# Kernel tuning notes

Hardware: AMD Instinct MI355X
Metric: run time of the kernel (lower is better)

The kernel has to match this reference:

```python
import jax, jax.numpy as jnp
import numpy as np


def setup_inputs() -> dict:
    key = jax.random.key(0)
    k1, k2 = jax.random.split(key)
    batch, cw_dim = 4096, 1024
    dim_embedding, book_size = 8, 256
    dim_codes = cw_dim // dim_embedding  # 128
    x = jax.random.normal(k1, (batch, cw_dim), dtype=jnp.float32)
    codebook = jax.random.normal(k2, (dim_codes, book_size, dim_embedding), dtype=jnp.float32)
    return {"x": x, "codebook": codebook}


def reference(x, codebook):
    # Faithful JAX version of VQVAE.quantise:
    #   pairwise squared distance -> argmin -> gather embeddings -> one-hot scatter
    C, K, D = codebook.shape          # dim_codes, book_size, dim_embedding
    B = x.shape[0]
    xr = x.reshape(B, C, D)           # [B, C, D] (= view(batch*dim_codes, 1, D))
    x2 = jnp.sum(xr * xr, axis=-1)                       # [B, C]
    c2 = jnp.sum(codebook * codebook, axis=-1)           # [C, K]
    dist = x2[..., None] - 2.0 * jnp.einsum('bcd,ckd->bck', xr, codebook) + c2[None]
    idx = jnp.argmin(dist, axis=-1)                      # [B, C]
    # gather nearest codebook entry per code slot
    cw_embed = codebook[jnp.arange(C)[None, :], idx]     # [B, C, D]
    cw_embed = cw_embed.reshape(B, C * D)                # [B, cw_dim]
    # one-hot scatter of selected indices
    one_hot_idx = jax.nn.one_hot(idx, K, dtype=jnp.float32)  # [B, C, K]
    return cw_embed, one_hot_idx
```

## Files before the change

kernel.cpp:

```cpp
#include <hip/hip_runtime.h>


constexpr int B_    = 4096;
constexpr int C_    = 128;
constexpr int K_    = 256;
constexpr int D_    = 8;
constexpr int TPB   = 256;
constexpr int BPT   = 4;
constexpr int BTILE = TPB * BPT;

__global__ __launch_bounds__(TPB, 2) void vq_argmin(
    const float* __restrict__ x,
    const float* __restrict__ cb,
    int* __restrict__ idx_out)
{
    __shared__ double s_cbd[K_ * D_];
    __shared__ double s_c2d[K_];

    const int c     = blockIdx.x;
    const int btile = blockIdx.y;
    const int tid   = threadIdx.x;

    {
        const float4* gcb = (const float4*)(cb + (size_t)c * (K_ * D_));
        const float4 v0 = gcb[tid];
        const float4 v1 = gcb[tid + TPB];
        const int i0 = tid * 4, i1 = (tid + TPB) * 4;
        s_cbd[i0 + 0] = (double)v0.x; s_cbd[i0 + 1] = (double)v0.y;
        s_cbd[i0 + 2] = (double)v0.z; s_cbd[i0 + 3] = (double)v0.w;
        s_cbd[i1 + 0] = (double)v1.x; s_cbd[i1 + 1] = (double)v1.y;
        s_cbd[i1 + 2] = (double)v1.z; s_cbd[i1 + 3] = (double)v1.w;
    }
    __syncthreads();

    {
        const double* v = s_cbd + tid * D_;
        double s = 0.0;
        #pragma unroll
        for (int d = 0; d < D_; ++d) s = fma(v[d], v[d], s);
        s_c2d[tid] = s;
    }
    __syncthreads();

    double xd[BPT][D_];
    #pragma unroll
    for (int j = 0; j < BPT; ++j) {
        const int b = btile * BTILE + j * TPB + tid;
        const float4* xp = (const float4*)(x + (size_t)b * (C_ * D_) + c * D_);
        const float4 a = xp[0];
        const float4 h = xp[1];
        xd[j][0] = (double)a.x; xd[j][1] = (double)a.y;
        xd[j][2] = (double)a.z; xd[j][3] = (double)a.w;
        xd[j][4] = (double)h.x; xd[j][5] = (double)h.y;
        xd[j][6] = (double)h.z; xd[j][7] = (double)h.w;
    }

    double best[BPT];
    int    bidx[BPT];
    #pragma unroll
    for (int j = 0; j < BPT; ++j) { best[j] = 1.0e300; bidx[j] = 0; }

    for (int k = 0; k < K_; ++k) {
        double cd[D_];
        #pragma unroll
        for (int d = 0; d < D_; ++d) cd[d] = s_cbd[k * D_ + d];
        const double c2k = s_c2d[k];
        #pragma unroll
        for (int j = 0; j < BPT; ++j) {
            double dot = xd[j][0] * cd[0];
            #pragma unroll
            for (int d = 1; d < D_; ++d) dot = fma(xd[j][d], cd[d], dot);
            const double score = fma(-2.0, dot, c2k);
            const bool lt = score < best[j];
            best[j] = lt ? score : best[j];
            bidx[j] = lt ? k : bidx[j];
        }
    }

    #pragma unroll
    for (int j = 0; j < BPT; ++j) {
        const int b = btile * BTILE + j * TPB + tid;
        idx_out[(size_t)b * C_ + c] = bidx[j];
    }
}

constexpr int GRID2 = 2048;
constexpr int RPB   = (B_ * C_) / GRID2;

__global__ __launch_bounds__(TPB, 4) void vq_write(
    const int*   __restrict__ idx,
    const float* __restrict__ cb,
    float* __restrict__ out_embed,
    float* __restrict__ out_onehot)
{
    const int tid  = threadIdx.x;
    const int lane = tid & 63;
    const int wave = tid >> 6;
    const int blk  = blockIdx.x;

    const int rowbase = blk * RPB + wave * 64;
    const int myk = idx[rowbase + lane];
    const int e0 = lane * 4;
    #pragma unroll 4
    for (int i = 0; i < 64; ++i) {
        const int k = __builtin_amdgcn_readlane(myk, i);
        float4 v;
        v.x = (k == e0    ) ? 1.f : 0.f;
        v.y = (k == e0 + 1) ? 1.f : 0.f;
        v.z = (k == e0 + 2) ? 1.f : 0.f;
        v.w = (k == e0 + 3) ? 1.f : 0.f;
        ((float4*)(out_onehot + (size_t)(rowbase + i) * K_))[lane] = v;
    }

    const size_t pbase = (size_t)blk * RPB;
    #pragma unroll
    for (int i = 0; i < 2; ++i) {
        const int    f    = i * TPB + tid;
        const int    pl   = f >> 1;
        const int    half = f & 1;
        const size_t pair = pbase + pl;
        const int    c    = (int)(pair & (C_ - 1));
        const int    k    = idx[pair];
        const float4 val  = ((const float4*)(cb + ((size_t)c * K_ + k) * D_))[half];
        ((float4*)(out_embed + pbase * D_))[f] = val;
    }
}

extern "C" void kernel_launch(void* const* d_in, const int* in_sizes, int n_in,
                              void* d_out, int out_size, void* d_ws, size_t ws_size,
                              hipStream_t stream) {
    const float* x  = (const float*)d_in[0];
    const float* cb = (const float*)d_in[1];
    float* out        = (float*)d_out;
    float* out_embed  = out;
    float* out_onehot = out + (size_t)B_ * C_ * D_;
    int*   idx_ws     = (int*)d_ws;

    dim3 grid1(C_, B_ / BTILE);
    vq_argmin<<<grid1, TPB, 0, stream>>>(x, cb, idx_ws);

    vq_write<<<GRID2, TPB, 0, stream>>>(idx_ws, cb, out_embed, out_onehot);
}
```

Measured before the change: 617.8 us.

## Screen argmin in fp32 and recheck near-tie pairs in fp64

Replaces the all-fp64 distance search with an fp32 pass that tracks both the best and second-best scores. Pairs whose margin falls under a small threshold are flagged in the sign bit, and a new fix-up kernel recomputes only those pairs in fp64 using a wave-wide reduction. The output writes also switch to nontemporal stores. This removes most of the slow fp64 arithmetic, at the cost of an extra launch and a threshold that could miss ties if fp32 error exceeds it.

```diff
diff --git a/kernel.cpp b/kernel.cpp
--- a/kernel.cpp
+++ b/kernel.cpp
@@ -1,21 +1,26 @@
 #include <hip/hip_runtime.h>
 
 
-constexpr int B_    = 4096;
-constexpr int C_    = 128;
-constexpr int K_    = 256;
-constexpr int D_    = 8;
-constexpr int TPB   = 256;
-constexpr int BPT   = 4;
-constexpr int BTILE = TPB * BPT;
-
-__global__ __launch_bounds__(TPB, 2) void vq_argmin(
+constexpr int B_  = 4096;
+constexpr int C_  = 128;
+constexpr int K_  = 256;
+constexpr int D_  = 8;
+constexpr int TPB = 256;
+constexpr int NP  = B_ * C_;
+
+typedef float  vf4 __attribute__((ext_vector_type(4)));
+
+constexpr int   BPT1   = 2;
+constexpr int   BTILE1 = TPB * BPT1;
+constexpr float TAU2   = 1.0e-3f;
+
+__global__ __launch_bounds__(TPB, 4) void vq_screen(
     const float* __restrict__ x,
     const float* __restrict__ cb,
     int* __restrict__ idx_out)
 {
-    __shared__ double s_cbd[K_ * D_];
-    __shared__ double s_c2d[K_];
+    __shared__ float s_cbf[K_ * D_];
+    __shared__ float s_c2f[K_];
 
     const int c     = blockIdx.x;
     const int btile = blockIdx.y;
@@ -23,69 +28,126 @@
 
     {
         const float4* gcb = (const float4*)(cb + (size_t)c * (K_ * D_));
-        const float4 v0 = gcb[tid];
-        const float4 v1 = gcb[tid + TPB];
-        const int i0 = tid * 4, i1 = (tid + TPB) * 4;
-        s_cbd[i0 + 0] = (double)v0.x; s_cbd[i0 + 1] = (double)v0.y;
-        s_cbd[i0 + 2] = (double)v0.z; s_cbd[i0 + 3] = (double)v0.w;
-        s_cbd[i1 + 0] = (double)v1.x; s_cbd[i1 + 1] = (double)v1.y;
-        s_cbd[i1 + 2] = (double)v1.z; s_cbd[i1 + 3] = (double)v1.w;
+        ((float4*)s_cbf)[tid]       = gcb[tid];
+        ((float4*)s_cbf)[tid + TPB] = gcb[tid + TPB];
     }
     __syncthreads();
-
     {
-        const double* v = s_cbd + tid * D_;
-        double s = 0.0;
+        const float* v = s_cbf + tid * D_;
+        float s = 0.f;
         #pragma unroll
-        for (int d = 0; d < D_; ++d) s = fma(v[d], v[d], s);
-        s_c2d[tid] = s;
+        for (int d = 0; d < D_; ++d) s = fmaf(v[d], v[d], s);
+        s_c2f[tid] = s;
     }
     __syncthreads();
 
-    double xd[BPT][D_];
-    #pragma unroll
-    for (int j = 0; j < BPT; ++j) {
-        const int b = btile * BTILE + j * TPB + tid;
+    float xf[BPT1][D_];
+    #pragma unroll
+    for (int j = 0; j < BPT1; ++j) {
+        const int b = btile * BTILE1 + j * TPB + tid;
         const float4* xp = (const float4*)(x + (size_t)b * (C_ * D_) + c * D_);
         const float4 a = xp[0];
         const float4 h = xp[1];
-        xd[j][0] = (double)a.x; xd[j][1] = (double)a.y;
-        xd[j][2] = (double)a.z; xd[j][3] = (double)a.w;
-        xd[j][4] = (double)h.x; xd[j][5] = (double)h.y;
-        xd[j][6] = (double)h.z; xd[j][7] = (double)h.w;
-    }
-
-    double best[BPT];
-    int    bidx[BPT];
-    #pragma unroll
-    for (int j = 0; j < BPT; ++j) { best[j] = 1.0e300; bidx[j] = 0; }
-
+        xf[j][0] = a.x; xf[j][1] = a.y; xf[j][2] = a.z; xf[j][3] = a.w;
+        xf[j][4] = h.x; xf[j][5] = h.y; xf[j][6] = h.z; xf[j][7] = h.w;
+    }
+
+    float s1[BPT1], s2[BPT1];
+    int   k1[BPT1];
+    #pragma unroll
+    for (int j = 0; j < BPT1; ++j) { s1[j] = 3.4e38f; s2[j] = 3.4e38f; k1[j] = 0; }
+
+    const float4* scb4 = (const float4*)s_cbf;
+    #pragma unroll 2
     for (int k = 0; k < K_; ++k) {
-        double cd[D_];
+        const float4 clo = scb4[k * 2];
+        const float4 chi = scb4[k * 2 + 1];
+        const float  c2k = s_c2f[k];
         #pragma unroll
-        for (int d = 0; d < D_; ++d) cd[d] = s_cbd[k * D_ + d];
-        const double c2k = s_c2d[k];
-        #pragma unroll
-        for (int j = 0; j < BPT; ++j) {
-            double dot = xd[j][0] * cd[0];
+        for (int j = 0; j < BPT1; ++j) {
+            float dot = xf[j][0] * clo.x;
+            dot = fmaf(xf[j][1], clo.y, dot);
+            dot = fmaf(xf[j][2], clo.z, dot);
+            dot = fmaf(xf[j][3], clo.w, dot);
+            dot = fmaf(xf[j][4], chi.x, dot);
+            dot = fmaf(xf[j][5], chi.y, dot);
+            dot = fmaf(xf[j][6], chi.z, dot);
+            dot = fmaf(xf[j][7], chi.w, dot);
+            const float score = fmaf(-2.f, dot, c2k);
+            s2[j] = fminf(s2[j], fmaxf(score, s1[j]));
+            const bool lt = score < s1[j];
+            k1[j] = lt ? k : k1[j];
+            s1[j] = lt ? score : s1[j];
+        }
+    }
+
+    #pragma unroll
+    for (int j = 0; j < BPT1; ++j) {
+        const int b = btile * BTILE1 + j * TPB + tid;
+        const bool amb = (s2[j] - s1[j]) <= TAU2;
+        idx_out[(size_t)b * C_ + c] = k1[j] | (amb ? (1 << 31) : 0);
+    }
+}
+
+constexpr int FIXBLKS = 256;
+
+__global__ __launch_bounds__(TPB, 4) void vq_fix(
+    const float* __restrict__ x,
+    const float* __restrict__ cb,
+    int* __restrict__ idx)
+{
+    const int lane   = threadIdx.x & 63;
+    const int gwave  = (blockIdx.x * TPB + threadIdx.x) >> 6;
+    const int nwaves = (FIXBLKS * TPB) >> 6;
+
+    for (int base = gwave * 64; base < NP; base += nwaves * 64) {
+        const int v = idx[base + lane];
+        unsigned long long mask = __ballot(v < 0);
+        while (mask) {
+            const int src = (int)__ffsll((long long)mask) - 1;
+            mask &= mask - 1;
+            const int pair = base + src;
+            const int b = pair >> 7;
+            const int c = pair & (C_ - 1);
+
+            const float* xp = x  + (size_t)b * (C_ * D_) + c * D_;
+            const float* cp = cb + (size_t)c * (K_ * D_);
+
+            double xd[D_];
             #pragma unroll
-            for (int d = 1; d < D_; ++d) dot = fma(xd[j][d], cd[d], dot);
-            const double score = fma(-2.0, dot, c2k);
-            const bool lt = score < best[j];
-            best[j] = lt ? score : best[j];
-            bidx[j] = lt ? k : bidx[j];
+            for (int d = 0; d < D_; ++d) xd[d] = (double)xp[d];
+
+            double best = 1.0e300;
+            int    bk   = 0;
+            #pragma unroll
+            for (int t = 0; t < 4; ++t) {
+                const int k = lane * 4 + t;
+                const float* cv = cp + k * D_;
+                double cd[D_];
+                #pragma unroll
+                for (int d = 0; d < D_; ++d) cd[d] = (double)cv[d];
+                double c2k = 0.0;
+                #pragma unroll
+                for (int d = 0; d < D_; ++d) c2k = fma(cd[d], cd[d], c2k);
+                double dot = xd[0] * cd[0];
+                #pragma unroll
+                for (int d = 1; d < D_; ++d) dot = fma(xd[d], cd[d], dot);
+                const double score = fma(-2.0, dot, c2k);
+                if (score < best) { best = score; bk = k; }
+            }
+            #pragma unroll
+            for (int off = 32; off >= 1; off >>= 1) {
+                const double ob  = __shfl_down(best, off);
+                const int    obk = __shfl_down(bk,   off);
+                if (ob < best) { best = ob; bk = obk; }
+            }
+            if (lane == 0) idx[pair] = bk;
         }
     }
-
-    #pragma unroll
-    for (int j = 0; j < BPT; ++j) {
-        const int b = btile * BTILE + j * TPB + tid;
-        idx_out[(size_t)b * C_ + c] = bidx[j];
-    }
-}
-
-constexpr int GRID2 = 2048;
-constexpr int RPB   = (B_ * C_) / GRID2;
+}
+
+constexpr int GRID3 = 2048;
+constexpr int RPB   = NP / GRID3;
 
 __global__ __launch_bounds__(TPB, 4) void vq_write(
     const int*   __restrict__ idx,
@@ -104,12 +166,13 @@
     #pragma unroll 4
     for (int i = 0; i < 64; ++i) {
         const int k = __builtin_amdgcn_readlane(myk, i);
-        float4 v;
+        vf4 v;
         v.x = (k == e0    ) ? 1.f : 0.f;
         v.y = (k == e0 + 1) ? 1.f : 0.f;
         v.z = (k == e0 + 2) ? 1.f : 0.f;
         v.w = (k == e0 + 3) ? 1.f : 0.f;
-        ((float4*)(out_onehot + (size_t)(rowbase + i) * K_))[lane] = v;
+        vf4* dst = (vf4*)(out_onehot + (size_t)(rowbase + i) * K_) + lane;
+        __builtin_nontemporal_store(v, dst);
     }
 
     const size_t pbase = (size_t)blk * RPB;
@@ -121,8 +184,8 @@
         const size_t pair = pbase + pl;
         const int    c    = (int)(pair & (C_ - 1));
         const int    k    = idx[pair];
-        const float4 val  = ((const float4*)(cb + ((size_t)c * K_ + k) * D_))[half];
-        ((float4*)(out_embed + pbase * D_))[f] = val;
+        const vf4 val = ((const vf4*)(cb + ((size_t)c * K_ + k) * D_))[half];
+        __builtin_nontemporal_store(val, (vf4*)(out_embed + pbase * D_) + f);
     }
 }
 
@@ -136,8 +199,10 @@
     float* out_onehot = out + (size_t)B_ * C_ * D_;
     int*   idx_ws     = (int*)d_ws;
 
-    dim3 grid1(C_, B_ / BTILE);
-    vq_argmin<<<grid1, TPB, 0, stream>>>(x, cb, idx_ws);
-
-    vq_write<<<GRID2, TPB, 0, stream>>>(idx_ws, cb, out_embed, out_onehot);
-}
+    dim3 grid1(C_, B_ / BTILE1);
+    vq_screen<<<grid1, TPB, 0, stream>>>(x, cb, idx_ws);
+
+    vq_fix<<<FIXBLKS, TPB, 0, stream>>>(x, cb, idx_ws);
+
+    vq_write<<<GRID3, TPB, 0, stream>>>(idx_ws, cb, out_embed, out_onehot);
+}
```

After: 602.9 us. 2.4% less time.
